# Performance work log

Measured on AMD Instinct MI355X. Metric: run time of the kernel, lower is better.

Reference implementation:

```python
import jax, jax.numpy as jnp
import numpy as np

N, K = 16384, 32          # num bboxes, context size
IN_F, HID = 608, 384      # in_features, hidden_dim
ALPHA = 0.2               # LeakyReLU slope
NEG_INF = -9e15


def setup_inputs() -> dict:
    key = jax.random.key(0)
    k1, k2, k3, k4, k5, k6, k7, k8 = jax.random.split(key, 8)
    h_i = jax.random.normal(k1, (N, IN_F), dtype=jnp.float32)
    idx = jax.random.randint(k2, (N, K), 0, N)
    pad = jax.random.uniform(k3, (N, K)) < 0.2
    context_indices = jnp.where(pad, -1, idx).astype(jnp.int64)
    s_in = 1.0 / np.sqrt(IN_F)
    s_a = 1.0 / np.sqrt(2 * HID)
    W_i = jax.random.uniform(k4, (IN_F, HID), minval=-s_in, maxval=s_in, dtype=jnp.float32)
    W_j = jax.random.uniform(k5, (IN_F, HID), minval=-s_in, maxval=s_in, dtype=jnp.float32)
    a_i = jax.random.uniform(k6, (HID,), minval=-s_a, maxval=s_a, dtype=jnp.float32)
    a_j = jax.random.uniform(k7, (HID,), minval=-s_a, maxval=s_a, dtype=jnp.float32)
    a_b = jax.random.uniform(k8, (1,), minval=-s_a, maxval=s_a, dtype=jnp.float32)
    return {"h_i": h_i, "context_indices": context_indices,
            "W_i": W_i, "W_j": W_j, "a_i": a_i, "a_j": a_j, "a_b": a_b}


def reference(h_i, context_indices, W_i, W_j, a_i, a_j, a_b):
    n = h_i.shape[0]
    Wh_i = h_i @ W_i                          # [N, H]
    # W_j has no bias, so projecting then gathering (zero pad row) equals
    # gathering zero-padded features then projecting.
    Wh_all = h_i @ W_j                        # [N, H]
    Wh_pad = jnp.concatenate([Wh_all, jnp.zeros((1, HID), Wh_all.dtype)], axis=0)
    idx = jnp.where(context_indices >= 0, context_indices, n)   # -1 -> zero row
    Wh_j = Wh_pad[idx]                        # [N, K, H] gather
    # attention_layer(concat(Wh_i, Wh_j)) == Wh_i@a_i + Wh_j@a_j + b
    scores = (Wh_i @ a_i)[:, None] + Wh_j @ a_j + a_b[0]        # [N, K]
    scores = jnp.where(scores > 0, scores, ALPHA * scores)      # LeakyReLU
    scores = jnp.where(context_indices >= 0, scores, NEG_INF)   # mask padding
    att = jax.nn.softmax(scores, axis=1)                        # [N, K]
    h_prime = jnp.einsum('nk,nkh->nh', att, Wh_j)               # [N, H]
    return h_prime
```

## Files before the change

kernel.cpp:

```cpp
#include <hip/hip_runtime.h>
#include <hip/hip_bf16.h>

typedef unsigned short u16;
typedef unsigned int u32;
typedef __attribute__((ext_vector_type(8))) __bf16 bf16x8;
typedef __attribute__((ext_vector_type(4))) __bf16 bf16x4;
typedef __attribute__((ext_vector_type(4))) float f32x4;

#define KCTX 32
#define INF_ 608
#define HID_ 384
#define NBOX 16384

#define WH_OFF  19922944
#define BT_OFF  32505856
#define V_OFF   32972800
#define SI_OFF  32975232
#define SJ_OFF  33040768
#define AJF_OFF 33106304
#define ABF_OFF 33107840

__device__ __forceinline__ float bfu(u16 u)  { return __uint_as_float(((u32)u) << 16); }
__device__ __forceinline__ float bflo(u32 u) { return __uint_as_float(u << 16); }
__device__ __forceinline__ float bfhi(u32 u) { return __uint_as_float(u & 0xffff0000u); }
__device__ __forceinline__ u16 f2bf(float x) {
  u32 u = __float_as_uint(x);
  return (u16)((u + 0x7fffu + ((u >> 16) & 1u)) >> 16);
}
__device__ __forceinline__ void async_ld16(const void* g, void* l) {
  __builtin_amdgcn_global_load_lds(
      (const __attribute__((address_space(1))) u32*)g,
      (__attribute__((address_space(3))) u32*)l, 16, 0, 0);
}

__device__ __forceinline__ int detect_f32(const u32* hw) {
  const u32 w = hw[threadIdx.x & 63];
  const int e = (int)((w >> 7) & 0xffu);
  const unsigned long long mb = __ballot(e > 134 || e < 100);
  return __popcll(mb) >= 16;
}
__device__ __forceinline__ int detect_i64(const int* ci) {
  const int hi = ci[2 * (threadIdx.x & 63) + 1];
  const unsigned long long mz = __ballot(hi == 0 || hi == -1);
  return __popcll(mz) >= 48;
}

__global__ __launch_bounds__(256) void prep_kernel(
    const void* __restrict__ h, const void* __restrict__ Wi,
    const void* __restrict__ Wj, const void* __restrict__ ai,
    const void* __restrict__ aj, const void* __restrict__ ab,
    u16* __restrict__ Bt, float* __restrict__ v,
    float* __restrict__ ajf, float* __restrict__ abf) {
  __shared__ u16 tile[64][65];
  const int f32m = detect_f32((const u32*)h);
  const int bid = blockIdx.x, tid = threadIdx.x;
  if (bid < 60) {
    const int ft = bid / 6, ht = bid - ft * 6;
    const int f0 = ft * 64, h0 = ht * 64;
    const int ln = tid & 63, fg = tid >> 6;
#pragma unroll
    for (int rr = 0; rr < 16; ++rr) {
      const int fl = fg * 16 + rr;
      const int f = f0 + fl;
      if (f < INF_)
        tile[fl][ln] = f32m ? f2bf(((const float*)Wj)[(size_t)f * HID_ + h0 + ln])
                            : ((const u16*)Wj)[(size_t)f * HID_ + h0 + ln];
    }
    __syncthreads();
#pragma unroll
    for (int rr = 0; rr < 16; ++rr) {
      const int hl = fg * 16 + rr;
      const int f = f0 + ln;
      if (f < INF_) Bt[(size_t)(h0 + hl) * INF_ + f] = tile[ln][hl];
    }
  } else if (bid < 98) {
    const int t = (bid - 60) * 16 + (tid >> 4);
    const int sl = tid & 15;
    if (t < INF_) {
      float s = 0.f;
      if (f32m) {
        const float4* wi = (const float4*)((const float*)Wi + (size_t)t * HID_);
        const float4* a4 = (const float4*)ai;
        for (int c = sl; c < 96; c += 16) {
          float4 x = wi[c], y = a4[c];
          s += x.x * y.x + x.y * y.y + x.z * y.z + x.w * y.w;
        }
      } else {
        const uint4* wi = (const uint4*)((const u16*)Wi + (size_t)t * HID_);
        const uint4* a4 = (const uint4*)ai;
        for (int c = sl; c < 48; c += 16) {
          uint4 x = wi[c], y = a4[c];
          s += bflo(x.x) * bflo(y.x) + bfhi(x.x) * bfhi(y.x)
             + bflo(x.y) * bflo(y.y) + bfhi(x.y) * bfhi(y.y)
             + bflo(x.z) * bflo(y.z) + bfhi(x.z) * bfhi(y.z)
             + bflo(x.w) * bflo(y.w) + bfhi(x.w) * bfhi(y.w);
        }
      }
      s += __shfl_xor(s, 1); s += __shfl_xor(s, 2);
      s += __shfl_xor(s, 4); s += __shfl_xor(s, 8);
      if (sl == 0) v[t] = s;
    }
  } else {
    for (int j = tid; j < HID_; j += 256)
      ajf[j] = f32m ? ((const float*)aj)[j] : bfu(((const u16*)aj)[j]);
    if (tid == 0)
      abf[0] = f32m ? ((const float*)ab)[0] : bfu(((const u16*)ab)[0]);
  }
}

__global__ __launch_bounds__(256) void gemm_fused(
    const void* __restrict__ A, const u16* __restrict__ Bt,
    const float* __restrict__ v, u16* __restrict__ C,
    float* __restrict__ si, const float* __restrict__ ajf,
    float* __restrict__ sj) {
  __shared__ __align__(16) u16 As[32][612];
  __shared__ __align__(16) u16 Bs[12288];
  const int f32m = detect_f32((const u32*)A);
  const int tid  = threadIdx.x;
  const int lane = tid & 63;
  const int wv   = tid >> 6;
  const int row0 = blockIdx.x * 32;
  const char* Btb = (const char*)Bt;

#pragma unroll
  for (int i = 0; i < 6; ++i) {
    const int c = tid + i * 256;
    async_ld16(Btb + (size_t)(c >> 2) * 1216 + (c & 3) * 16, (char*)Bs + c * 16);
  }

  {
    const int g = tid >> 3, sub = tid & 7;
    float s = 0.f;
    const float4* v4 = (const float4*)v;
    if (f32m) {
      const float4* hr = (const float4*)((const float*)A + (size_t)(row0 + g) * INF_);
#pragma unroll
      for (int k = 0; k < 19; ++k) {
        const int c4 = sub + 8 * k;
        float4 x = hr[c4];
        ushort4 sv;
        sv.x = f2bf(x.x); sv.y = f2bf(x.y); sv.z = f2bf(x.z); sv.w = f2bf(x.w);
        *(ushort4*)&As[g][c4 * 4] = sv;
        float4 w = v4[c4];
        s += x.x * w.x + x.y * w.y + x.z * w.z + x.w * w.w;
      }
    } else {
      const uint4* hr = (const uint4*)((const u16*)A + (size_t)(row0 + g) * INF_);
      for (int k = 0; k < 10; ++k) {
        const int c8 = sub + 8 * k;
        if (c8 < 76) {
          uint4 x = hr[c8];
          *(ushort4*)&As[g][c8 * 8]     = *(ushort4*)&x.x;
          *(ushort4*)&As[g][c8 * 8 + 4] = *(ushort4*)&x.z;
          float4 w0 = v4[2 * c8], w1 = v4[2 * c8 + 1];
          s += bflo(x.x) * w0.x + bfhi(x.x) * w0.y + bflo(x.y) * w0.z + bfhi(x.y) * w0.w
             + bflo(x.z) * w1.x + bfhi(x.z) * w1.y + bflo(x.w) * w1.z + bfhi(x.w) * w1.w;
        }
      }
    }
    s += __shfl_xor(s, 1); s += __shfl_xor(s, 2); s += __shfl_xor(s, 4);
    if (sub == 0) si[row0 + g] = s;
  }

  f32x4 acc[2][6];
#pragma unroll
  for (int i = 0; i < 2; ++i)
#pragma unroll
    for (int j = 0; j < 6; ++j) acc[i][j] = (f32x4){0.f, 0.f, 0.f, 0.f};

  const int lm = lane & 15, q = lane >> 4;
  const int n0 = wv * 96;

  for (int kt = 0; kt < 19; ++kt) {
    __syncthreads();
    bf16x8 af[2], bfr[6];
#pragma unroll
    for (int im = 0; im < 2; ++im) {
      const int r = im * 16 + lm;
      bf16x4 lo = *(const bf16x4*)&As[r][kt * 32 + q * 8];
      bf16x4 hi = *(const bf16x4*)&As[r][kt * 32 + q * 8 + 4];
      af[im] = __builtin_shufflevector(lo, hi, 0, 1, 2, 3, 4, 5, 6, 7);
    }
#pragma unroll
    for (int in = 0; in < 6; ++in)
      bfr[in] = *(const bf16x8*)&Bs[(n0 + in * 16 + lm) * 32 + q * 8];
#pragma unroll
    for (int im = 0; im < 2; ++im)
#pragma unroll
      for (int in = 0; in < 6; ++in)
        acc[im][in] = __builtin_amdgcn_mfma_f32_16x16x32_bf16(
            af[im], bfr[in], acc[im][in], 0, 0, 0);
    __syncthreads();
    if (kt < 18) {
      const size_t kb = (size_t)(kt + 1) * 64;
#pragma unroll
      for (int i = 0; i < 6; ++i) {
        const int c = tid + i * 256;
        async_ld16(Btb + (size_t)(c >> 2) * 1216 + kb + (c & 3) * 16, (char*)Bs + c * 16);
      }
    }
  }

#pragma unroll
  for (int im = 0; im < 2; ++im)
#pragma unroll
    for (int in = 0; in < 6; ++in) {
      const int colg = n0 + in * 16 + lm;
#pragma unroll
      for (int r = 0; r < 4; ++r) {
        const int rowg = row0 + im * 16 + q * 4 + r;
        C[(size_t)rowg * HID_ + colg] = f2bf(acc[im][in][r]);
      }
    }
  float* sjred = (float*)Bs;
  float ajv[6];
#pragma unroll
  for (int in = 0; in < 6; ++in) ajv[in] = ajf[n0 + in * 16 + lm];
#pragma unroll
  for (int im = 0; im < 2; ++im)
#pragma unroll
    for (int r = 0; r < 4; ++r) {
      float p = acc[im][0][r] * ajv[0] + acc[im][1][r] * ajv[1]
              + acc[im][2][r] * ajv[2] + acc[im][3][r] * ajv[3]
              + acc[im][4][r] * ajv[4] + acc[im][5][r] * ajv[5];
      p += __shfl_xor(p, 1); p += __shfl_xor(p, 2);
      p += __shfl_xor(p, 4); p += __shfl_xor(p, 8);
      if (lm == 0) sjred[wv * 32 + im * 16 + q * 4 + r] = p;
    }
  __syncthreads();
  if (tid < 32)
    sj[row0 + tid] = sjred[tid] + sjred[32 + tid] + sjred[64 + tid] + sjred[96 + tid];
}

__global__ __launch_bounds__(256) void attn_kernel(
    const void* __restrict__ h, const int* __restrict__ ci,
    const float* __restrict__ si, const float* __restrict__ sj,
    const float* __restrict__ abf, const u16* __restrict__ Wh,
    void* __restrict__ out) {
  __shared__ float2 ai_c[5][32];
  __shared__ int cnt_s[5];
  const int f32m = detect_f32((const u32*)h);
  const int i64  = detect_i64(ci);
  const int tid = threadIdx.x;
  const int n0 = blockIdx.x * 5;

  if (tid < 160) {
    const int r = tid >> 5, k = tid & 31;
    const int n = n0 + r;
    if (n < NBOX) {
      const size_t t = (size_t)n * KCTX + k;
      int idx;
      if (i64) { int lo = ci[2 * t], hi2 = ci[2 * t + 1]; idx = (hi2 < 0) ? -1 : lo; }
      else     { idx = ci[t]; }
      const bool valid = idx >= 0;
      const float sjv = valid ? sj[idx] : 0.f;
      float raw = si[n] + sjv + abf[0];
      float lr = raw > 0.f ? raw : 0.2f * raw;
      float s = valid ? lr : -9e15f;
      float m = s;
#pragma unroll
      for (int o = 16; o; o >>= 1) m = fmaxf(m, __shfl_xor(m, o, 32));
      float p = __expf(s - m);
      float d = p;
#pragma unroll
      for (int o = 16; o; o >>= 1) d += __shfl_xor(d, o, 32);
      float w = p / d;
      unsigned key = valid ? (unsigned)idx : 0x7fffffffu;
#pragma unroll
      for (int kk = 2; kk <= 32; kk <<= 1) {
#pragma unroll
        for (int j = kk >> 1; j > 0; j >>= 1) {
          unsigned pk = __shfl_xor(key, j, 32);
          float    pw = __shfl_xor(w,   j, 32);
          const bool want_min = ((k & kk) == 0) == ((k & j) == 0);
          const bool take = want_min ? (pk < key) : (pk > key);
          if (take) { key = pk; w = pw; }
        }
      }
      const unsigned long long bm = __ballot(valid);
      const u32 m32 = (u32)(bm >> (tid & 32));
      const int cnt = __popc(m32);
      const int r8 = (cnt + 7) & ~7;
      ai_c[r][k] = (k < cnt) ? (float2){w, __int_as_float((int)key)}
                             : (float2){0.f, 0.f};
      if (k == 0) cnt_s[r] = r8;
    } else if ((tid & 31) == 0) {
      cnt_s[r] = 0;
    }
  }
  __syncthreads();

  if (tid < 240) {
    const int r = tid / 48, c = tid - r * 48;
    const int n = n0 + r;
    if (n < NBOX) {
      const int K8 = cnt_s[r];
      float a0 = 0, a1 = 0, a2 = 0, a3 = 0, a4 = 0, a5 = 0, a6 = 0, a7 = 0;
      for (int kb = 0; kb < K8; kb += 8) {
        uint4 q[8]; float ww[8];
#pragma unroll
        for (int u = 0; u < 8; ++u) {
          const float2 e = ai_c[r][kb + u];
          ww[u] = e.x;
          const int j = __float_as_int(e.y);
          q[u] = ((const uint4*)(Wh + (u32)j * HID_))[c];
        }
#pragma unroll
        for (int u = 0; u < 8; ++u) {
          const float w = ww[u];
          a0 += w * bflo(q[u].x); a1 += w * bfhi(q[u].x);
          a2 += w * bflo(q[u].y); a3 += w * bfhi(q[u].y);
          a4 += w * bflo(q[u].z); a5 += w * bfhi(q[u].z);
          a6 += w * bflo(q[u].w); a7 += w * bfhi(q[u].w);
        }
      }
      if (f32m) {
        float4* o4 = (float4*)out + (size_t)n * 96 + c * 2;
        o4[0] = (float4){a0, a1, a2, a3};
        o4[1] = (float4){a4, a5, a6, a7};
      } else {
        uint4 o;
        o.x = (u32)f2bf(a0) | ((u32)f2bf(a1) << 16);
        o.y = (u32)f2bf(a2) | ((u32)f2bf(a3) << 16);
        o.z = (u32)f2bf(a4) | ((u32)f2bf(a5) << 16);
        o.w = (u32)f2bf(a6) | ((u32)f2bf(a7) << 16);
        ((uint4*)out)[(size_t)n * 48 + c] = o;
      }
    }
  }
}

extern "C" void kernel_launch(void* const* d_in, const int* in_sizes, int n_in,
                              void* d_out, int out_size, void* d_ws, size_t ws_size,
                              hipStream_t stream) {
  const void* h  = d_in[0];
  const int*  ci = (const int*)d_in[1];
  const void* Wi = d_in[2];
  const void* Wj = d_in[3];
  const void* ai = d_in[4];
  const void* aj = d_in[5];
  const void* ab = d_in[6];

  char* ws = (char*)d_ws;
  u16*   Wh  = (u16*)(ws + WH_OFF);
  u16*   Bt  = (u16*)(ws + BT_OFF);
  float* v   = (float*)(ws + V_OFF);
  float* si  = (float*)(ws + SI_OFF);
  float* sj  = (float*)(ws + SJ_OFF);
  float* ajf = (float*)(ws + AJF_OFF);
  float* abf = (float*)(ws + ABF_OFF);

  prep_kernel<<<99, 256, 0, stream>>>(h, Wi, Wj, ai, aj, ab, Bt, v, ajf, abf);
  gemm_fused<<<512, 256, 0, stream>>>(h, Bt, v, Wh, si, ajf, sj);
  attn_kernel<<<3277, 256, 0, stream>>>(h, ci, si, sj, abf, Wh, d_out);
}
```

Baseline: 156.6 us.

## Double-buffer B tiles in 64-row 512-thread GEMM blocks and fence attn load scheduling

The fused projection GEMM now processes 64 rows per block with 8 waves, using dynamic shared memory. Each wave owns 48 output columns across 4 row tiles. The B tile is double-buffered so the next K-slice is prefetched before the MFMAs on the current one, which drops one barrier per iteration. The larger footprint (about 127KB LDS) limits residency to one block per CU and halves the grid. A sched_barrier in the attention gather loop keeps all gathered loads issued before the FMA block.

```diff
diff --git a/kernel.cpp b/kernel.cpp
--- a/kernel.cpp
+++ b/kernel.cpp
@@ -108,23 +108,25 @@
   }
 }
 
-__global__ __launch_bounds__(256) void gemm_fused(
+#define ASRO 612
+__global__ __launch_bounds__(512, 2) void gemm_fused(
     const void* __restrict__ A, const u16* __restrict__ Bt,
     const float* __restrict__ v, u16* __restrict__ C,
     float* __restrict__ si, const float* __restrict__ ajf,
     float* __restrict__ sj) {
-  __shared__ __align__(16) u16 As[32][612];
-  __shared__ __align__(16) u16 Bs[12288];
+  extern __shared__ __align__(16) char smem[];
+  u16* As = (u16*)smem;
+  u16* Bs = (u16*)(smem + 78336);
   const int f32m = detect_f32((const u32*)A);
   const int tid  = threadIdx.x;
   const int lane = tid & 63;
   const int wv   = tid >> 6;
-  const int row0 = blockIdx.x * 32;
+  const int row0 = blockIdx.x * 64;
   const char* Btb = (const char*)Bt;
 
 #pragma unroll
-  for (int i = 0; i < 6; ++i) {
-    const int c = tid + i * 256;
+  for (int i = 0; i < 3; ++i) {
+    const int c = tid + i * 512;
     async_ld16(Btb + (size_t)(c >> 2) * 1216 + (c & 3) * 16, (char*)Bs + c * 16);
   }
 
@@ -140,7 +142,7 @@
         float4 x = hr[c4];
         ushort4 sv;
         sv.x = f2bf(x.x); sv.y = f2bf(x.y); sv.z = f2bf(x.z); sv.w = f2bf(x.w);
-        *(ushort4*)&As[g][c4 * 4] = sv;
+        *(ushort4*)&As[g * ASRO + c4 * 4] = sv;
         float4 w = v4[c4];
         s += x.x * w.x + x.y * w.y + x.z * w.z + x.w * w.w;
       }
@@ -150,8 +152,8 @@
         const int c8 = sub + 8 * k;
         if (c8 < 76) {
           uint4 x = hr[c8];
-          *(ushort4*)&As[g][c8 * 8]     = *(ushort4*)&x.x;
-          *(ushort4*)&As[g][c8 * 8 + 4] = *(ushort4*)&x.z;
+          *(ushort4*)&As[g * ASRO + c8 * 8]     = *(ushort4*)&x.x;
+          *(ushort4*)&As[g * ASRO + c8 * 8 + 4] = *(ushort4*)&x.z;
           float4 w0 = v4[2 * c8], w1 = v4[2 * c8 + 1];
           s += bflo(x.x) * w0.x + bfhi(x.x) * w0.y + bflo(x.y) * w0.z + bfhi(x.y) * w0.w
              + bflo(x.z) * w1.x + bfhi(x.z) * w1.y + bflo(x.w) * w1.z + bfhi(x.w) * w1.w;
@@ -162,49 +164,52 @@
     if (sub == 0) si[row0 + g] = s;
   }
 
-  f32x4 acc[2][6];
-#pragma unroll
-  for (int i = 0; i < 2; ++i)
-#pragma unroll
-    for (int j = 0; j < 6; ++j) acc[i][j] = (f32x4){0.f, 0.f, 0.f, 0.f};
+  f32x4 acc[4][3];
+#pragma unroll
+  for (int i = 0; i < 4; ++i)
+#pragma unroll
+    for (int j = 0; j < 3; ++j) acc[i][j] = (f32x4){0.f, 0.f, 0.f, 0.f};
 
   const int lm = lane & 15, q = lane >> 4;
-  const int n0 = wv * 96;
-
+  const int n0 = wv * 48;
+
+  __syncthreads();
+  int cur = 0;
   for (int kt = 0; kt < 19; ++kt) {
-    __syncthreads();
-    bf16x8 af[2], bfr[6];
-#pragma unroll
-    for (int im = 0; im < 2; ++im) {
+    if (kt < 18) {
+      const size_t kb = (size_t)(kt + 1) * 64;
+#pragma unroll
+      for (int i = 0; i < 3; ++i) {
+        const int c = tid + i * 512;
+        async_ld16(Btb + (size_t)(c >> 2) * 1216 + kb + (c & 3) * 16,
+                   (char*)Bs + (cur ^ 1) * 24576 + c * 16);
+      }
+    }
+    bf16x8 af[4], bfr[3];
+#pragma unroll
+    for (int im = 0; im < 4; ++im) {
       const int r = im * 16 + lm;
-      bf16x4 lo = *(const bf16x4*)&As[r][kt * 32 + q * 8];
-      bf16x4 hi = *(const bf16x4*)&As[r][kt * 32 + q * 8 + 4];
+      bf16x4 lo = *(const bf16x4*)&As[r * ASRO + kt * 32 + q * 8];
+      bf16x4 hi = *(const bf16x4*)&As[r * ASRO + kt * 32 + q * 8 + 4];
       af[im] = __builtin_shufflevector(lo, hi, 0, 1, 2, 3, 4, 5, 6, 7);
     }
 #pragma unroll
-    for (int in = 0; in < 6; ++in)
-      bfr[in] = *(const bf16x8*)&Bs[(n0 + in * 16 + lm) * 32 + q * 8];
-#pragma unroll
-    for (int im = 0; im < 2; ++im)
-#pragma unroll
-      for (int in = 0; in < 6; ++in)
+    for (int in = 0; in < 3; ++in)
+      bfr[in] = *(const bf16x8*)&Bs[cur * 12288 + (n0 + in * 16 + lm) * 32 + q * 8];
+#pragma unroll
+    for (int im = 0; im < 4; ++im)
+#pragma unroll
+      for (int in = 0; in < 3; ++in)
         acc[im][in] = __builtin_amdgcn_mfma_f32_16x16x32_bf16(
             af[im], bfr[in], acc[im][in], 0, 0, 0);
     __syncthreads();
-    if (kt < 18) {
-      const size_t kb = (size_t)(kt + 1) * 64;
-#pragma unroll
-      for (int i = 0; i < 6; ++i) {
-        const int c = tid + i * 256;
-        async_ld16(Btb + (size_t)(c >> 2) * 1216 + kb + (c & 3) * 16, (char*)Bs + c * 16);
-      }
-    }
-  }
-
-#pragma unroll
-  for (int im = 0; im < 2; ++im)
-#pragma unroll
-    for (int in = 0; in < 6; ++in) {
+    cur ^= 1;
+  }
+
+#pragma unroll
+  for (int im = 0; im < 4; ++im)
+#pragma unroll
+    for (int in = 0; in < 3; ++in) {
       const int colg = n0 + in * 16 + lm;
 #pragma unroll
       for (int r = 0; r < 4; ++r) {
@@ -213,23 +218,26 @@
       }
     }
   float* sjred = (float*)Bs;
-  float ajv[6];
-#pragma unroll
-  for (int in = 0; in < 6; ++in) ajv[in] = ajf[n0 + in * 16 + lm];
-#pragma unroll
-  for (int im = 0; im < 2; ++im)
+  float ajv[3];
+#pragma unroll
+  for (int in = 0; in < 3; ++in) ajv[in] = ajf[n0 + in * 16 + lm];
+#pragma unroll
+  for (int im = 0; im < 4; ++im)
 #pragma unroll
     for (int r = 0; r < 4; ++r) {
       float p = acc[im][0][r] * ajv[0] + acc[im][1][r] * ajv[1]
-              + acc[im][2][r] * ajv[2] + acc[im][3][r] * ajv[3]
-              + acc[im][4][r] * ajv[4] + acc[im][5][r] * ajv[5];
+              + acc[im][2][r] * ajv[2];
       p += __shfl_xor(p, 1); p += __shfl_xor(p, 2);
       p += __shfl_xor(p, 4); p += __shfl_xor(p, 8);
-      if (lm == 0) sjred[wv * 32 + im * 16 + q * 4 + r] = p;
+      if (lm == 0) sjred[wv * 64 + im * 16 + q * 4 + r] = p;
     }
   __syncthreads();
-  if (tid < 32)
-    sj[row0 + tid] = sjred[tid] + sjred[32 + tid] + sjred[64 + tid] + sjred[96 + tid];
+  if (tid < 64) {
+    float s = 0.f;
+#pragma unroll
+    for (int w = 0; w < 8; ++w) s += sjred[w * 64 + tid];
+    sj[row0 + tid] = s;
+  }
 }
 
 __global__ __launch_bounds__(256) void attn_kernel(
@@ -305,6 +313,7 @@
           const int j = __float_as_int(e.y);
           q[u] = ((const uint4*)(Wh + (u32)j * HID_))[c];
         }
+        __builtin_amdgcn_sched_barrier(0);
 #pragma unroll
         for (int u = 0; u < 8; ++u) {
           const float w = ww[u];
@@ -351,6 +360,6 @@
   float* abf = (float*)(ws + ABF_OFF);
 
   prep_kernel<<<99, 256, 0, stream>>>(h, Wi, Wj, ai, aj, ab, Bt, v, ajf, abf);
-  gemm_fused<<<512, 256, 0, stream>>>(h, Bt, v, Wh, si, ajf, sj);
+  gemm_fused<<<256, 512, 127488, stream>>>(h, Bt, v, Wh, si, ajf, sj);
   attn_kernel<<<3277, 256, 0, stream>>>(h, ci, si, sj, abf, Wh, d_out);
 }
```

Measured after the change: 157.7 us. No clear change (+0.7%).
